# Kernel optimization log

Hardware: AMD Instinct MI355X
Metric: run time of the kernel (lower is better)

Reference implementation:

```python
import jax, jax.numpy as jnp
import numpy as np

B, S, D, H = 4, 4096, 512, 2
PD = D // H  # projection_dim = 256


def setup_inputs() -> dict:
    key = jax.random.key(0)
    ks = jax.random.split(key, 6)
    scale = 1.0 / np.sqrt(D)
    return {
        "x": jax.random.normal(ks[0], (B, S, D), dtype=jnp.float32),
        "Wq": jax.random.normal(ks[1], (D, D), dtype=jnp.float32) * scale,
        "bq": jnp.zeros((D,), dtype=jnp.float32),
        "Wk": jax.random.normal(ks[2], (D, D), dtype=jnp.float32) * scale,
        "bk": jnp.zeros((D,), dtype=jnp.float32),
        "Wv": jax.random.normal(ks[3], (D, D), dtype=jnp.float32) * scale,
        "bv": jnp.zeros((D,), dtype=jnp.float32),
        "Wo": jax.random.normal(ks[4], (D, D), dtype=jnp.float32) * scale,
        "bo": jnp.zeros((D,), dtype=jnp.float32),
    }


def _split_heads(t):
    # [B, S, D] -> [B, H, S, PD]
    return t.reshape(B, S, H, PD).transpose(0, 2, 1, 3)


def reference(x, Wq, bq, Wk, bk, Wv, bv, Wo, bo):
    Q = _split_heads(x @ Wq + bq)
    K = _split_heads(x @ Wk + bk)
    V = _split_heads(x @ Wv + bv)
    # scaled dot-product attention, non-causal (no mask in original)
    scores = jnp.einsum("bhqd,bhkd->bhqk", Q, K) / jnp.sqrt(jnp.float32(PD))
    weights = jax.nn.softmax(scores, axis=-1)
    attn = jnp.einsum("bhqk,bhkd->bhqd", weights, V)
    # merge heads: [B, H, S, PD] -> [B, S, D]
    concat = attn.transpose(0, 2, 1, 3).reshape(B, S, D)
    return concat @ Wo + bo
```

## Files before the change

kernel.cpp:

```cpp
#include <hip/hip_runtime.h>
#include <hip/hip_bf16.h>


#define B_  4
#define S_  4096
#define D_  512
#define H_  2
#define PD_ 256
#define QSCALE 0.09016844f

typedef __attribute__((ext_vector_type(4))) float f32x4;
typedef __attribute__((ext_vector_type(16))) float f32x16;
typedef __attribute__((ext_vector_type(8))) short short8;
typedef __attribute__((ext_vector_type(4))) short short4v;
typedef __attribute__((ext_vector_type(4))) unsigned u32x4;

static __device__ __forceinline__ short f2bf(float f) {
  unsigned u = __float_as_uint(f);
  u += 0x7fffu + ((u >> 16) & 1u);
  return (short)(u >> 16);
}
static __device__ __forceinline__ unsigned cvtpk(float a, float b) {
  unsigned r;
  asm("v_cvt_pk_bf16_f32 %0, %1, %2" : "=v"(r) : "v"(a), "v"(b));
  return r;
}
static __device__ __forceinline__ void gload16(const short* g, const short* l) {
  __builtin_amdgcn_global_load_lds((const __attribute__((address_space(1))) void*)g,
                                   (__attribute__((address_space(3))) void*)l,
                                   16, 0, 0);
}

__global__ void convert_x_kernel(const float* __restrict__ x, short* __restrict__ xb, int n8) {
  int i = blockIdx.x * blockDim.x + threadIdx.x;
  int stride = gridDim.x * blockDim.x;
  for (; i < n8; i += stride) {
    const f32x4* p = (const f32x4*)(x + (size_t)i * 8);
    f32x4 a = p[0], b = p[1];
    short8 v;
    v[0] = f2bf(a[0]); v[1] = f2bf(a[1]); v[2] = f2bf(a[2]); v[3] = f2bf(a[3]);
    v[4] = f2bf(b[0]); v[5] = f2bf(b[1]); v[6] = f2bf(b[2]); v[7] = f2bf(b[3]);
    *(short8*)(xb + (size_t)i * 8) = v;
  }
}

__global__ __launch_bounds__(256) void transpose_w(
    const float* __restrict__ W0, const float* __restrict__ W1,
    const float* __restrict__ W2, const float* __restrict__ W3,
    short* __restrict__ T0, short* __restrict__ T1,
    short* __restrict__ T2, short* __restrict__ T3) {
  const float* W = (blockIdx.z == 0) ? W0 : (blockIdx.z == 1) ? W1 : (blockIdx.z == 2) ? W2 : W3;
  short* T = (blockIdx.z == 0) ? T0 : (blockIdx.z == 1) ? T1 : (blockIdx.z == 2) ? T2 : T3;
  __shared__ float tile[32][33];
  int tx = threadIdx.x & 31, ty = threadIdx.x >> 5;
  int r0 = blockIdx.x * 32, c0 = blockIdx.y * 32;
#pragma unroll
  for (int i = 0; i < 4; ++i)
    tile[ty + 8 * i][tx] = W[(size_t)(r0 + ty + 8 * i) * D_ + c0 + tx];
  __syncthreads();
#pragma unroll
  for (int i = 0; i < 4; ++i)
    T[(size_t)(c0 + ty + 8 * i) * D_ + r0 + tx] = f2bf(tile[tx][ty + 8 * i]);
}

__global__ __launch_bounds__(256) void transpose_v(
    const short* __restrict__ Vw, short* __restrict__ Vt) {
  __shared__ short tile[64][68];
  int h = blockIdx.z;
  int s0 = blockIdx.x * 64, d0 = blockIdx.y * 64;
  const short* src = Vw + (size_t)h * S_ * PD_;
  short* dst = Vt + (size_t)h * S_ * PD_;
  int tx = threadIdx.x & 15, ty = threadIdx.x >> 4;
#pragma unroll
  for (int i = 0; i < 4; ++i) {
    short4v v = *(const short4v*)(src + (size_t)(s0 + ty + 16 * i) * PD_ + d0 + tx * 4);
    *(short4v*)&tile[ty + 16 * i][tx * 4] = v;
  }
  __syncthreads();
#pragma unroll
  for (int i = 0; i < 4; ++i) {
    int d = d0 + ty + 16 * i;
    short4v v;
#pragma unroll
    for (int j = 0; j < 4; ++j) v[j] = tile[tx * 4 + j][ty + 16 * i];
    int swz = ((tx >> 1) & 3) ^ ((d >> 3) & 3);
    *(short4v*)(dst + (size_t)d * S_ + s0 + (tx >> 3) * 32 + swz * 8 + (tx & 1) * 4) = v;
  }
}

template <int MODE>
__global__ __launch_bounds__(256, 2) void gemm_bt(
    const short* __restrict__ A,
    const short* __restrict__ Bt0, const short* __restrict__ Bt1, const short* __restrict__ Bt2,
    const float* __restrict__ b0, const float* __restrict__ b1, const float* __restrict__ b2,
    short* __restrict__ o0, short* __restrict__ o1, short* __restrict__ o2,
    float* __restrict__ fout) {
  __shared__ short sA[128 * 72];
  __shared__ short sB[128 * 72];

  const int tid = threadIdx.x;
  const int lane = tid & 63, wid = tid >> 6;
  const int wr = wid >> 1, wc = wid & 1;
  const int l15 = lane & 15, g = lane >> 4;
  const int m0 = blockIdx.x * 128, n0 = blockIdx.y * 128;

  const short* Bt = (MODE == 0) ? ((blockIdx.z == 0) ? Bt0 : (blockIdx.z == 1) ? Bt1 : Bt2) : Bt0;
  const float* bias = (MODE == 0) ? ((blockIdx.z == 0) ? b0 : (blockIdx.z == 1) ? b1 : b2) : b0;

  short8 pa[4], pb[4];

  auto loadT = [&](int kt) {
#pragma unroll
    for (int i = 0; i < 4; ++i) {
      int slot = tid + 256 * i;
      int r = slot >> 3, gg = slot & 7;
      pa[i] = *(const short8*)(A + (size_t)(m0 + r) * D_ + kt * 64 + 8 * gg);
      pb[i] = *(const short8*)(Bt + (size_t)(n0 + r) * D_ + kt * 64 + 8 * gg);
    }
  };
  auto storeT = [&]() {
#pragma unroll
    for (int i = 0; i < 4; ++i) {
      int slot = tid + 256 * i;
      int r = slot >> 3, gg = slot & 7;
      *(short8*)&sA[r * 72 + 8 * gg] = pa[i];
      *(short8*)&sB[r * 72 + 8 * gg] = pb[i];
    }
  };

  f32x4 acc[4][4];
#pragma unroll
  for (int i = 0; i < 4; ++i)
#pragma unroll
    for (int j = 0; j < 4; ++j) acc[i][j] = (f32x4)0.0f;

  loadT(0);
#pragma unroll 1
  for (int kt = 0; kt < 8; ++kt) {
    __syncthreads();
    storeT();
    if (kt < 7) loadT(kt + 1);
    __syncthreads();
#pragma unroll
    for (int s = 0; s < 2; ++s) {
      short8 a[4], b[4];
#pragma unroll
      for (int fr = 0; fr < 4; ++fr)
        a[fr] = *(const short8*)&sA[(wr * 64 + fr * 16 + l15) * 72 + 32 * s + 8 * g];
#pragma unroll
      for (int fc = 0; fc < 4; ++fc)
        b[fc] = *(const short8*)&sB[(wc * 64 + fc * 16 + l15) * 72 + 32 * s + 8 * g];
#pragma unroll
      for (int fr = 0; fr < 4; ++fr)
#pragma unroll
        for (int fc = 0; fc < 4; ++fc)
          acc[fr][fc] = __builtin_amdgcn_mfma_f32_16x16x32_bf16(a[fr], b[fc], acc[fr][fc], 0, 0, 0);
    }
  }

  if (MODE == 0) {
    short* dst = (blockIdx.z == 0) ? o0 : (blockIdx.z == 1) ? o1 : o2;
    const bool kswz = (blockIdx.z == 1);
    const float sc = (blockIdx.z == 0) ? QSCALE : 1.0f;
#pragma unroll
    for (int fc = 0; fc < 4; ++fc) {
      int n = n0 + wc * 64 + fc * 16 + l15;
      float bvv = bias[n];
      int h = n >> 8, pd = n & 255;
#pragma unroll
      for (int fr = 0; fr < 4; ++fr)
#pragma unroll
        for (int r = 0; r < 4; ++r) {
          int m = m0 + wr * 64 + fr * 16 + 4 * g + r;
          int bb = m >> 12, ss = m & 4095;
          int pdw = pd;
          if (kswz) {
            int ch = pd >> 3;
            pdw = (pd & 7) | (((ch & 24) | ((ch & 7) ^ (ss & 7))) << 3);
          }
          dst[((size_t)((bb * H_ + h) * S_ + ss)) * PD_ + pdw] = f2bf((acc[fr][fc][r] + bvv) * sc);
        }
    }
  } else {
#pragma unroll
    for (int fc = 0; fc < 4; ++fc) {
      int n = n0 + wc * 64 + fc * 16 + l15;
      float bvv = bias[n];
#pragma unroll
      for (int fr = 0; fr < 4; ++fr)
#pragma unroll
        for (int r = 0; r < 4; ++r) {
          int m = m0 + wr * 64 + fr * 16 + 4 * g + r;
          fout[(size_t)m * D_ + n] = acc[fr][fc][r] + bvv;
        }
    }
  }
}

__global__ __launch_bounds__(512, 2) void attn4_kernel(
    const short* __restrict__ Qw, const short* __restrict__ Kw,
    const short* __restrict__ Vt, short* __restrict__ ATT) {
  __shared__ __align__(16) char smem[133120];
  __shared__ float sMm[8][32];
  __shared__ float sB1[8][32];
  __shared__ float sMl[4][32];

  const int tid = threadIdx.x, lane = tid & 63, w = tid >> 6;
  const int l31 = lane & 31, hi = lane >> 5;
  const int head = blockIdx.x & 7, qb = blockIdx.x >> 3;
  const int kh = w >> 2, qg = w & 3;
  const size_t hoff = (size_t)head * S_ * PD_;
  const short* Qh = Qw + hoff;
  const short* Kh = Kw + hoff;
  const short* Vh = Vt + hoff;

  const int qrow = qb * 128 + qg * 32 + l31;
  short8 qf[16];
#pragma unroll
  for (int dc = 0; dc < 16; ++dc)
    qf[dc] = *(const short8*)(Qh + (size_t)qrow * PD_ + dc * 16 + hi * 8);

  const int mm = l31 & 7, pp = (l31 >> 1) & 3, q3 = l31 >> 3;
  int kaddr[4];
#pragma unroll
  for (int b = 0; b < 4; ++b)
    kaddr[b] = kh * 32768 + l31 * 512 + ((b ^ pp) << 5) + ((hi ^ (mm & 1)) << 4);
  int vaddr[2];
#pragma unroll
  for (int c = 0; c < 2; ++c)
    vaddr[c] = 65536 + kh * 32768 + l31 * 64 + (((2 * c + hi) ^ q3) << 4);

  f32x16 o[8];
#pragma unroll
  for (int i = 0; i < 8; ++i) o[i] = (f32x16)0.0f;
  float mrun = -3.0e38f, lrun = 0.0f;

  auto stage = [&](int buf, int t) {
    const short* kt = Kh + (size_t)(t * 32) * PD_;
#pragma unroll
    for (int i = 0; i < 4; ++i) {
      int s = tid + 512 * i;
      int half = s >> 10, s1 = s & 1023;
      gload16(kt + (size_t)(half * 2048) * PD_ + (s1 >> 5) * PD_ + (s1 & 31) * 8,
              (const short*)(smem + half * 32768 + buf * 16384 + s1 * 16));
    }
    const short* vt = Vh + t * 32;
#pragma unroll
    for (int i = 0; i < 4; ++i) {
      int s = tid + 512 * i;
      int half = s >> 10, s1 = s & 1023;
      gload16(vt + (size_t)(s1 >> 2) * S_ + half * 2048 + (s1 & 3) * 8,
              (const short*)(smem + 65536 + half * 32768 + buf * 16384 + s1 * 16));
    }
  };

  auto compute = [&](int buf) {
    f32x16 sa = (f32x16)0.0f, sb = (f32x16)0.0f;
#pragma unroll
    for (int a = 0; a < 4; ++a)
#pragma unroll
      for (int b = 0; b < 4; ++b) {
        short8 kf = *(const short8*)(smem + kaddr[b] + a * 128 + buf * 16384);
        if (a < 2)
          sa = __builtin_amdgcn_mfma_f32_32x32x16_bf16(kf, qf[4 * a + b], sa, 0, 0, 0);
        else
          sb = __builtin_amdgcn_mfma_f32_32x32x16_bf16(kf, qf[4 * a + b], sb, 0, 0, 0);
      }
    f32x16 sacc = sa + sb;

    float tmax = fmaxf(sacc[0], sacc[1]);
#pragma unroll
    for (int r = 2; r < 16; ++r) tmax = fmaxf(tmax, sacc[r]);
    tmax = fmaxf(tmax, __shfl_xor(tmax, 32));
    if (!__all(tmax <= mrun + 8.0f)) {
      float mn = fmaxf(mrun, tmax);
      float resc = exp2f(mrun - mn);
      mrun = mn;
      lrun *= resc;
      if (!hi) sB1[w][l31] = resc;
      asm volatile("" ::: "memory");
      f32x4 rv0 = *(const f32x4*)&sB1[w][0 + hi * 4];
      f32x4 rv1 = *(const f32x4*)&sB1[w][8 + hi * 4];
      f32x4 rv2 = *(const f32x4*)&sB1[w][16 + hi * 4];
      f32x4 rv3 = *(const f32x4*)&sB1[w][24 + hi * 4];
#pragma unroll
      for (int dcb = 0; dcb < 8; ++dcb)
#pragma unroll
        for (int r = 0; r < 16; ++r) {
          float rr = (r < 4 ? rv0 : r < 8 ? rv1 : r < 12 ? rv2 : rv3)[r & 3];
          o[dcb][r] *= rr;
        }
    }
    float lsum = 0.0f;
#pragma unroll
    for (int r = 0; r < 16; ++r) {
      float pv = exp2f(sacc[r] - mrun);
      sacc[r] = pv;
      lsum += pv;
    }
    lsum += __shfl_xor(lsum, 32);
    lrun += lsum;

#pragma unroll
    for (int c = 0; c < 2; ++c) {
      unsigned pk0 = cvtpk(sacc[8 * c + 0], sacc[8 * c + 1]);
      unsigned pk1 = cvtpk(sacc[8 * c + 2], sacc[8 * c + 3]);
      unsigned pk2 = cvtpk(sacc[8 * c + 4], sacc[8 * c + 5]);
      unsigned pk3 = cvtpk(sacc[8 * c + 6], sacc[8 * c + 7]);
      unsigned sh0 = __shfl_xor(pk0, 32);
      unsigned sh1 = __shfl_xor(pk1, 32);
      unsigned sh2 = __shfl_xor(pk2, 32);
      unsigned sh3 = __shfl_xor(pk3, 32);
      u32x4 ua;
      ua[0] = hi ? sh2 : pk0;
      ua[1] = hi ? sh3 : pk1;
      ua[2] = hi ? pk2 : sh0;
      ua[3] = hi ? pk3 : sh1;
      short8 af = *(short8*)&ua;
#pragma unroll
      for (int dcb = 0; dcb < 8; ++dcb) {
        short8 vf = *(const short8*)(smem + vaddr[c] + dcb * 2048 + buf * 16384);
        o[dcb] = __builtin_amdgcn_mfma_f32_32x32x16_bf16(af, vf, o[dcb], 0, 0, 0);
      }
    }
  };

  stage(0, 0);
#pragma unroll 1
  for (int t = 0; t < 64; t += 2) {
    __syncthreads();
    stage(1, t + 1);
    compute(0);
    __syncthreads();
    if (t + 2 < 64) stage(0, t + 2);
    compute(1);
  }

  __syncthreads();
  if (!hi) sMm[w][l31] = mrun;
  __syncthreads();
  {
    float mo = sMm[w ^ 4][l31];
    float mf = fmaxf(mrun, mo);
    float sc = exp2f(mrun - mf);
    lrun *= sc;
    if (!hi) sB1[w][l31] = sc;
    asm volatile("" ::: "memory");
    f32x4 rv0 = *(const f32x4*)&sB1[w][0 + hi * 4];
    f32x4 rv1 = *(const f32x4*)&sB1[w][8 + hi * 4];
    f32x4 rv2 = *(const f32x4*)&sB1[w][16 + hi * 4];
    f32x4 rv3 = *(const f32x4*)&sB1[w][24 + hi * 4];
#pragma unroll
    for (int dcb = 0; dcb < 8; ++dcb)
#pragma unroll
      for (int r = 0; r < 16; ++r) {
        float rr = (r < 4 ? rv0 : r < 8 ? rv1 : r < 12 ? rv2 : rv3)[r & 3];
        o[dcb][r] *= rr;
      }
    if (w >= 4 && !hi) sMl[w - 4][l31] = lrun;
  }
  __syncthreads();
  float* mb = (float*)smem;
  if (w >= 4) {
    float* rg = mb + (size_t)qg * 8320;
#pragma unroll
    for (int dcb = 0; dcb < 8; ++dcb)
#pragma unroll
      for (int r4 = 0; r4 < 4; ++r4) {
        f32x4 v;
        v[0] = o[dcb][4 * r4 + 0];
        v[1] = o[dcb][4 * r4 + 1];
        v[2] = o[dcb][4 * r4 + 2];
        v[3] = o[dcb][4 * r4 + 3];
        *(f32x4*)&rg[(size_t)(dcb * 4 + r4) * 260 + lane * 4] = v;
      }
  }
  __syncthreads();
  if (w < 4) {
    float* rg = mb + (size_t)qg * 8320;
#pragma unroll
    for (int dcb = 0; dcb < 8; ++dcb)
#pragma unroll
      for (int r4 = 0; r4 < 4; ++r4) {
        f32x4 v = *(const f32x4*)&rg[(size_t)(dcb * 4 + r4) * 260 + lane * 4];
        o[dcb][4 * r4 + 0] += v[0];
        o[dcb][4 * r4 + 1] += v[1];
        o[dcb][4 * r4 + 2] += v[2];
        o[dcb][4 * r4 + 3] += v[3];
      }
    lrun += sMl[qg][l31];
    if (!hi) sB1[w][l31] = 1.0f / lrun;
    asm volatile("" ::: "memory");
    f32x4 iv0 = *(const f32x4*)&sB1[w][0 + hi * 4];
    f32x4 iv1 = *(const f32x4*)&sB1[w][8 + hi * 4];
    f32x4 iv2 = *(const f32x4*)&sB1[w][16 + hi * 4];
    f32x4 iv3 = *(const f32x4*)&sB1[w][24 + hi * 4];
    const int bb = head >> 1, hh = head & 1;
#pragma unroll
    for (int r = 0; r < 16; ++r) {
      int q = qb * 128 + qg * 32 + (r & 3) + 8 * (r >> 2) + 4 * hi;
      float iv = (r < 4 ? iv0 : r < 8 ? iv1 : r < 12 ? iv2 : iv3)[r & 3];
      size_t base = ((size_t)(bb * S_ + q)) * D_ + hh * PD_;
#pragma unroll
      for (int dcb = 0; dcb < 8; ++dcb)
        ATT[base + dcb * 32 + l31] = f2bf(o[dcb][r] * iv);
    }
  }
}

extern "C" void kernel_launch(void* const* d_in, const int* in_sizes, int n_in,
                              void* d_out, int out_size, void* d_ws, size_t ws_size,
                              hipStream_t stream) {
  const float* x  = (const float*)d_in[0];
  const float* Wq = (const float*)d_in[1];
  const float* bq = (const float*)d_in[2];
  const float* Wk = (const float*)d_in[3];
  const float* bk = (const float*)d_in[4];
  const float* Wv = (const float*)d_in[5];
  const float* bv = (const float*)d_in[6];
  const float* Wo = (const float*)d_in[7];
  const float* bo = (const float*)d_in[8];
  float* out = (float*)d_out;

  char* ws = (char*)d_ws;
  const size_t WSZ = (size_t)D_ * D_ * 2;
  const size_t QSZ = (size_t)B_ * H_ * S_ * PD_ * 2;
  short* wtq = (short*)(ws);
  short* wtk = (short*)(ws + WSZ);
  short* wtv = (short*)(ws + 2 * WSZ);
  short* wto = (short*)(ws + 3 * WSZ);
  short* Qw  = (short*)(ws + 4 * WSZ);
  short* Kw  = (short*)(ws + 4 * WSZ + QSZ);
  short* Vw  = (short*)(ws + 4 * WSZ + 2 * QSZ);
  short* ATT = (short*)(ws + 4 * WSZ + 3 * QSZ);
  short* XB  = ATT;
  short* Vtp = (short*)d_out;

  convert_x_kernel<<<dim3(2048), dim3(256), 0, stream>>>(x, XB, (B_ * S_ * D_) / 8);
  transpose_w<<<dim3(16, 16, 4), dim3(256), 0, stream>>>(Wq, Wk, Wv, Wo, wtq, wtk, wtv, wto);
  gemm_bt<0><<<dim3(128, 4, 3), dim3(256), 0, stream>>>(
      XB, wtq, wtk, wtv, bq, bk, bv, Qw, Kw, Vw, (float*)nullptr);
  transpose_v<<<dim3(64, 4, 8), dim3(256), 0, stream>>>(Vw, Vtp);
  attn4_kernel<<<dim3(256), dim3(512), 0, stream>>>(Qw, Kw, Vtp, ATT);
  gemm_bt<1><<<dim3(128, 4, 1), dim3(256), 0, stream>>>(
      ATT, wto, wto, wto, bo, bo, bo, nullptr, nullptr, nullptr, out);
}
```

Measured before the change: 290.2 us.

## Software-pipeline attention: overlap next QK^T with current softmax and PV

Restructures the attention main loop so the QK^T MFMAs for the next key tile are issued before the softmax and PV of the previous tile, using double-buffered K and triple-buffered V in a larger LDS allocation. There is one barrier per tile instead of two. MFMA sections are wrapped in s_setprio to favour matrix issue, and row-rescale factors are broadcast with lane shuffles instead of LDS round-trips. This aims to hide softmax latency and barrier stalls behind matrix work. The cost is more registers for two score accumulators and 160KB of LDS, which risks occupancy or spills under the 2-block launch bound.

```diff
diff --git a/kernel.cpp b/kernel.cpp
--- a/kernel.cpp
+++ b/kernel.cpp
@@ -197,13 +197,10 @@
   }
 }
 
-__global__ __launch_bounds__(512, 2) void attn4_kernel(
+__global__ __launch_bounds__(512, 2) void attn6_kernel(
     const short* __restrict__ Qw, const short* __restrict__ Kw,
     const short* __restrict__ Vt, short* __restrict__ ATT) {
-  __shared__ __align__(16) char smem[133120];
-  __shared__ float sMm[8][32];
-  __shared__ float sB1[8][32];
-  __shared__ float sMl[4][32];
+  __shared__ __align__(16) char smem[163840];
 
   const int tid = threadIdx.x, lane = tid & 63, w = tid >> 6;
   const int l31 = lane & 31, hi = lane >> 5;
@@ -211,7 +208,6 @@
   const int kh = w >> 2, qg = w & 3;
   const size_t hoff = (size_t)head * S_ * PD_;
   const short* Qh = Qw + hoff;
-  const short* Kh = Kw + hoff;
   const short* Vh = Vt + hoff;
 
   const int qrow = qb * 128 + qg * 32 + l31;
@@ -224,188 +220,205 @@
   int kaddr[4];
 #pragma unroll
   for (int b = 0; b < 4; ++b)
-    kaddr[b] = kh * 32768 + l31 * 512 + ((b ^ pp) << 5) + ((hi ^ (mm & 1)) << 4);
+    kaddr[b] = kh * 16384 + l31 * 512 + ((b ^ pp) << 5) + ((hi ^ (mm & 1)) << 4);
   int vaddr[2];
 #pragma unroll
   for (int c = 0; c < 2; ++c)
-    vaddr[c] = 65536 + kh * 32768 + l31 * 64 + (((2 * c + hi) ^ q3) << 4);
+    vaddr[c] = kh * 16384 + l31 * 64 + (((2 * c + hi) ^ q3) << 4);
+
+  const int lk0 = tid * 16;
+  const int gk0 = (tid >> 5) * PD_ + (tid & 31) * 8;
+  const int gv0 = (tid >> 2) * S_ + (tid & 3) * 8;
+  const short* kg = Kw + hoff;
+  const short* vg = Vh;
 
   f32x16 o[8];
 #pragma unroll
   for (int i = 0; i < 8; ++i) o[i] = (f32x16)0.0f;
+  f32x16 sA, sB;
   float mrun = -3.0e38f, lrun = 0.0f;
 
-  auto stage = [&](int buf, int t) {
-    const short* kt = Kh + (size_t)(t * 32) * PD_;
-#pragma unroll
-    for (int i = 0; i < 4; ++i) {
-      int s = tid + 512 * i;
-      int half = s >> 10, s1 = s & 1023;
-      gload16(kt + (size_t)(half * 2048) * PD_ + (s1 >> 5) * PD_ + (s1 & 31) * 8,
-              (const short*)(smem + half * 32768 + buf * 16384 + s1 * 16));
-    }
-    const short* vt = Vh + t * 32;
-#pragma unroll
-    for (int i = 0; i < 4; ++i) {
-      int s = tid + 512 * i;
-      int half = s >> 10, s1 = s & 1023;
-      gload16(vt + (size_t)(s1 >> 2) * S_ + half * 2048 + (s1 & 3) * 8,
-              (const short*)(smem + 65536 + half * 32768 + buf * 16384 + s1 * 16));
-    }
-  };
-
-  auto compute = [&](int buf) {
-    f32x16 sa = (f32x16)0.0f, sb = (f32x16)0.0f;
-#pragma unroll
-    for (int a = 0; a < 4; ++a)
-#pragma unroll
-      for (int b = 0; b < 4; ++b) {
-        short8 kf = *(const short8*)(smem + kaddr[b] + a * 128 + buf * 16384);
-        if (a < 2)
-          sa = __builtin_amdgcn_mfma_f32_32x32x16_bf16(kf, qf[4 * a + b], sa, 0, 0, 0);
-        else
-          sb = __builtin_amdgcn_mfma_f32_32x32x16_bf16(kf, qf[4 * a + b], sb, 0, 0, 0);
-      }
-    f32x16 sacc = sa + sb;
-
-    float tmax = fmaxf(sacc[0], sacc[1]);
-#pragma unroll
-    for (int r = 2; r < 16; ++r) tmax = fmaxf(tmax, sacc[r]);
-    tmax = fmaxf(tmax, __shfl_xor(tmax, 32));
-    if (!__all(tmax <= mrun + 8.0f)) {
-      float mn = fmaxf(mrun, tmax);
-      float resc = exp2f(mrun - mn);
-      mrun = mn;
-      lrun *= resc;
-      if (!hi) sB1[w][l31] = resc;
-      asm volatile("" ::: "memory");
-      f32x4 rv0 = *(const f32x4*)&sB1[w][0 + hi * 4];
-      f32x4 rv1 = *(const f32x4*)&sB1[w][8 + hi * 4];
-      f32x4 rv2 = *(const f32x4*)&sB1[w][16 + hi * 4];
-      f32x4 rv3 = *(const f32x4*)&sB1[w][24 + hi * 4];
-#pragma unroll
-      for (int dcb = 0; dcb < 8; ++dcb)
-#pragma unroll
-        for (int r = 0; r < 16; ++r) {
-          float rr = (r < 4 ? rv0 : r < 8 ? rv1 : r < 12 ? rv2 : rv3)[r & 3];
-          o[dcb][r] *= rr;
-        }
-    }
-    float lsum = 0.0f;
-#pragma unroll
-    for (int r = 0; r < 16; ++r) {
-      float pv = exp2f(sacc[r] - mrun);
-      sacc[r] = pv;
-      lsum += pv;
-    }
-    lsum += __shfl_xor(lsum, 32);
-    lrun += lsum;
-
-#pragma unroll
-    for (int c = 0; c < 2; ++c) {
-      unsigned pk0 = cvtpk(sacc[8 * c + 0], sacc[8 * c + 1]);
-      unsigned pk1 = cvtpk(sacc[8 * c + 2], sacc[8 * c + 3]);
-      unsigned pk2 = cvtpk(sacc[8 * c + 4], sacc[8 * c + 5]);
-      unsigned pk3 = cvtpk(sacc[8 * c + 6], sacc[8 * c + 7]);
-      unsigned sh0 = __shfl_xor(pk0, 32);
-      unsigned sh1 = __shfl_xor(pk1, 32);
-      unsigned sh2 = __shfl_xor(pk2, 32);
-      unsigned sh3 = __shfl_xor(pk3, 32);
-      u32x4 ua;
-      ua[0] = hi ? sh2 : pk0;
-      ua[1] = hi ? sh3 : pk1;
-      ua[2] = hi ? pk2 : sh0;
-      ua[3] = hi ? pk3 : sh1;
-      short8 af = *(short8*)&ua;
-#pragma unroll
-      for (int dcb = 0; dcb < 8; ++dcb) {
-        short8 vf = *(const short8*)(smem + vaddr[c] + dcb * 2048 + buf * 16384);
-        o[dcb] = __builtin_amdgcn_mfma_f32_32x32x16_bf16(af, vf, o[dcb], 0, 0, 0);
-      }
-    }
-  };
-
-  stage(0, 0);
+#define STAGE_K(KN)                                                                  \
+  gload16(kg + gk0,          (const short*)(smem + (KN) * 32768 + lk0));             \
+  gload16(kg + gk0 + 4096,   (const short*)(smem + (KN) * 32768 + 8192 + lk0));      \
+  gload16(kg + gk0 + 524288, (const short*)(smem + (KN) * 32768 + 16384 + lk0));     \
+  gload16(kg + gk0 + 528384, (const short*)(smem + (KN) * 32768 + 24576 + lk0));
+
+#define STAGE_V(VS)                                                                  \
+  gload16(vg + gv0,          (const short*)(smem + 65536 + (VS) * 32768 + lk0));     \
+  gload16(vg + gv0 + 524288, (const short*)(smem + 65536 + (VS) * 32768 + 8192 + lk0)); \
+  gload16(vg + gv0 + 2048,   (const short*)(smem + 65536 + (VS) * 32768 + 16384 + lk0)); \
+  gload16(vg + gv0 + 526336, (const short*)(smem + 65536 + (VS) * 32768 + 24576 + lk0));
+
+#define QK_(SCUR, KC)                                                                \
+  {                                                                                  \
+    f32x16 _a = (f32x16)0.0f, _b = (f32x16)0.0f;                                     \
+    __builtin_amdgcn_s_setprio(1);                                                   \
+    _Pragma("unroll")                                                                \
+    for (int a = 0; a < 4; ++a) {                                                    \
+      _Pragma("unroll")                                                              \
+      for (int b = 0; b < 4; ++b) {                                                  \
+        short8 kf = *(const short8*)(smem + (KC) * 32768 + kaddr[b] + a * 128);      \
+        if (b & 1) _b = __builtin_amdgcn_mfma_f32_32x32x16_bf16(kf, qf[4 * a + b], _b, 0, 0, 0); \
+        else       _a = __builtin_amdgcn_mfma_f32_32x32x16_bf16(kf, qf[4 * a + b], _a, 0, 0, 0); \
+      }                                                                              \
+    }                                                                                \
+    __builtin_amdgcn_s_setprio(0);                                                   \
+    SCUR = _a + _b;                                                                  \
+  }
+
+#define SM_(S)                                                                       \
+  {                                                                                  \
+    float t0 = fmaxf(S[0], S[1]),   t1 = fmaxf(S[2], S[3]);                          \
+    float t2 = fmaxf(S[4], S[5]),   t3 = fmaxf(S[6], S[7]);                          \
+    float t4 = fmaxf(S[8], S[9]),   t5 = fmaxf(S[10], S[11]);                        \
+    float t6 = fmaxf(S[12], S[13]), t7 = fmaxf(S[14], S[15]);                        \
+    t0 = fmaxf(t0, t1); t2 = fmaxf(t2, t3); t4 = fmaxf(t4, t5); t6 = fmaxf(t6, t7);  \
+    t0 = fmaxf(t0, t2); t4 = fmaxf(t4, t6);                                          \
+    float tmax = fmaxf(t0, t4);                                                      \
+    tmax = fmaxf(tmax, __shfl_xor(tmax, 32));                                        \
+    if (!__all(tmax <= mrun + 8.0f)) {                                               \
+      float mn = fmaxf(mrun, tmax);                                                  \
+      float resc = exp2f(mrun - mn);                                                 \
+      mrun = mn; lrun *= resc;                                                       \
+      _Pragma("unroll")                                                              \
+      for (int r = 0; r < 16; ++r) {                                                 \
+        float rr = __shfl(resc, (r & 3) + 8 * (r >> 2) + 4 * hi, 64);                \
+        _Pragma("unroll")                                                            \
+        for (int d = 0; d < 8; ++d) o[d][r] *= rr;                                   \
+      }                                                                              \
+    }                                                                                \
+    _Pragma("unroll")                                                                \
+    for (int r = 0; r < 16; ++r) S[r] = exp2f(S[r] - mrun);                          \
+    float u0 = (S[0] + S[1]) + (S[2] + S[3]);                                        \
+    float u1 = (S[4] + S[5]) + (S[6] + S[7]);                                        \
+    u0 += (S[8] + S[9]) + (S[10] + S[11]);                                           \
+    u1 += (S[12] + S[13]) + (S[14] + S[15]);                                         \
+    float ls = u0 + u1;                                                              \
+    ls += __shfl_xor(ls, 32);                                                        \
+    lrun += ls;                                                                      \
+  }
+
+#define PV_(S, VP)                                                                   \
+  {                                                                                  \
+    _Pragma("unroll")                                                                \
+    for (int c = 0; c < 2; ++c) {                                                    \
+      unsigned pk0 = cvtpk(S[8 * c + 0], S[8 * c + 1]);                              \
+      unsigned pk1 = cvtpk(S[8 * c + 2], S[8 * c + 3]);                              \
+      unsigned pk2 = cvtpk(S[8 * c + 4], S[8 * c + 5]);                              \
+      unsigned pk3 = cvtpk(S[8 * c + 6], S[8 * c + 7]);                              \
+      unsigned sh0 = __shfl_xor(pk0, 32);                                            \
+      unsigned sh1 = __shfl_xor(pk1, 32);                                            \
+      unsigned sh2 = __shfl_xor(pk2, 32);                                            \
+      unsigned sh3 = __shfl_xor(pk3, 32);                                            \
+      u32x4 ua;                                                                      \
+      ua[0] = hi ? sh2 : pk0;                                                        \
+      ua[1] = hi ? sh3 : pk1;                                                        \
+      ua[2] = hi ? pk2 : sh0;                                                        \
+      ua[3] = hi ? pk3 : sh1;                                                        \
+      short8 af = *(short8*)&ua;                                                     \
+      __builtin_amdgcn_s_setprio(1);                                                 \
+      _Pragma("unroll")                                                              \
+      for (int d = 0; d < 8; ++d) {                                                  \
+        short8 vf = *(const short8*)(smem + 65536 + (VP) * 32768 + vaddr[c] + d * 2048); \
+        o[d] = __builtin_amdgcn_mfma_f32_32x32x16_bf16(af, vf, o[d], 0, 0, 0);       \
+      }                                                                              \
+      __builtin_amdgcn_s_setprio(0);                                                 \
+    }                                                                                \
+  }
+
+#define REGION(KC, KN, VP, VS, SCUR, SPRV, DOSTAGE)                                  \
+  __syncthreads();                                                                   \
+  if (DOSTAGE) { STAGE_K(KN); STAGE_V(VS); }                                         \
+  kg += 32 * PD_; vg += 32;                                                          \
+  QK_(SCUR, KC);                                                                     \
+  SM_(SPRV);                                                                         \
+  PV_(SPRV, VP);
+
+  STAGE_K(0); STAGE_V(0);
+  kg += 32 * PD_; vg += 32;
+  __syncthreads();
+  STAGE_K(1); STAGE_V(1);
+  kg += 32 * PD_; vg += 32;
+  QK_(sA, 0);
+
 #pragma unroll 1
-  for (int t = 0; t < 64; t += 2) {
-    __syncthreads();
-    stage(1, t + 1);
-    compute(0);
-    __syncthreads();
-    if (t + 2 < 64) stage(0, t + 2);
-    compute(1);
-  }
-
-  __syncthreads();
-  if (!hi) sMm[w][l31] = mrun;
+  for (int it = 0; it < 10; ++it) {
+    REGION(1, 0, 0, 2, sB, sA, 1)
+    REGION(0, 1, 1, 0, sA, sB, 1)
+    REGION(1, 0, 2, 1, sB, sA, 1)
+    REGION(0, 1, 0, 2, sA, sB, 1)
+    REGION(1, 0, 1, 0, sB, sA, 1)
+    REGION(0, 1, 2, 1, sA, sB, 1)
+  }
+  REGION(1, 0, 0, 2, sB, sA, 1)
+  REGION(0, 1, 1, 0, sA, sB, 1)
+  REGION(1, 0, 2, 1, sB, sA, 0)
+  SM_(sB);
+  PV_(sB, 0);
+
+  __syncthreads();
+  float* sMm = (float*)smem;
+  float* sMl = (float*)(smem + 1024);
+  float* dep = (float*)(smem + 4096);
+  if (!hi) sMm[w * 32 + l31] = mrun;
   __syncthreads();
   {
-    float mo = sMm[w ^ 4][l31];
+    float mo = sMm[(w ^ 4) * 32 + l31];
     float mf = fmaxf(mrun, mo);
     float sc = exp2f(mrun - mf);
     lrun *= sc;
-    if (!hi) sB1[w][l31] = sc;
-    asm volatile("" ::: "memory");
-    f32x4 rv0 = *(const f32x4*)&sB1[w][0 + hi * 4];
-    f32x4 rv1 = *(const f32x4*)&sB1[w][8 + hi * 4];
-    f32x4 rv2 = *(const f32x4*)&sB1[w][16 + hi * 4];
-    f32x4 rv3 = *(const f32x4*)&sB1[w][24 + hi * 4];
-#pragma unroll
-    for (int dcb = 0; dcb < 8; ++dcb)
-#pragma unroll
-      for (int r = 0; r < 16; ++r) {
-        float rr = (r < 4 ? rv0 : r < 8 ? rv1 : r < 12 ? rv2 : rv3)[r & 3];
-        o[dcb][r] *= rr;
-      }
-    if (w >= 4 && !hi) sMl[w - 4][l31] = lrun;
-  }
-  __syncthreads();
-  float* mb = (float*)smem;
+#pragma unroll
+    for (int r = 0; r < 16; ++r) {
+      float rr = __shfl(sc, (r & 3) + 8 * (r >> 2) + 4 * hi, 64);
+#pragma unroll
+      for (int d = 0; d < 8; ++d) o[d][r] *= rr;
+    }
+    if (w >= 4 && !hi) sMl[(w - 4) * 32 + l31] = lrun;
+  }
+  __syncthreads();
   if (w >= 4) {
-    float* rg = mb + (size_t)qg * 8320;
-#pragma unroll
-    for (int dcb = 0; dcb < 8; ++dcb)
+    float* rg = dep + (size_t)qg * 8320;
+#pragma unroll
+    for (int d = 0; d < 8; ++d)
 #pragma unroll
       for (int r4 = 0; r4 < 4; ++r4) {
         f32x4 v;
-        v[0] = o[dcb][4 * r4 + 0];
-        v[1] = o[dcb][4 * r4 + 1];
-        v[2] = o[dcb][4 * r4 + 2];
-        v[3] = o[dcb][4 * r4 + 3];
-        *(f32x4*)&rg[(size_t)(dcb * 4 + r4) * 260 + lane * 4] = v;
+#pragma unroll
+        for (int j = 0; j < 4; ++j) v[j] = o[d][4 * r4 + j];
+        *(f32x4*)&rg[(size_t)(d * 4 + r4) * 260 + lane * 4] = v;
       }
   }
   __syncthreads();
   if (w < 4) {
-    float* rg = mb + (size_t)qg * 8320;
-#pragma unroll
-    for (int dcb = 0; dcb < 8; ++dcb)
+    float* rg = dep + (size_t)qg * 8320;
+#pragma unroll
+    for (int d = 0; d < 8; ++d)
 #pragma unroll
       for (int r4 = 0; r4 < 4; ++r4) {
-        f32x4 v = *(const f32x4*)&rg[(size_t)(dcb * 4 + r4) * 260 + lane * 4];
-        o[dcb][4 * r4 + 0] += v[0];
-        o[dcb][4 * r4 + 1] += v[1];
-        o[dcb][4 * r4 + 2] += v[2];
-        o[dcb][4 * r4 + 3] += v[3];
+        f32x4 v = *(const f32x4*)&rg[(size_t)(d * 4 + r4) * 260 + lane * 4];
+#pragma unroll
+        for (int j = 0; j < 4; ++j) o[d][4 * r4 + j] += v[j];
       }
-    lrun += sMl[qg][l31];
-    if (!hi) sB1[w][l31] = 1.0f / lrun;
-    asm volatile("" ::: "memory");
-    f32x4 iv0 = *(const f32x4*)&sB1[w][0 + hi * 4];
-    f32x4 iv1 = *(const f32x4*)&sB1[w][8 + hi * 4];
-    f32x4 iv2 = *(const f32x4*)&sB1[w][16 + hi * 4];
-    f32x4 iv3 = *(const f32x4*)&sB1[w][24 + hi * 4];
+    lrun += sMl[qg * 32 + l31];
+    float inv = 1.0f / lrun;
     const int bb = head >> 1, hh = head & 1;
 #pragma unroll
     for (int r = 0; r < 16; ++r) {
       int q = qb * 128 + qg * 32 + (r & 3) + 8 * (r >> 2) + 4 * hi;
-      float iv = (r < 4 ? iv0 : r < 8 ? iv1 : r < 12 ? iv2 : iv3)[r & 3];
+      float iv = __shfl(inv, (r & 3) + 8 * (r >> 2) + 4 * hi, 64);
       size_t base = ((size_t)(bb * S_ + q)) * D_ + hh * PD_;
 #pragma unroll
-      for (int dcb = 0; dcb < 8; ++dcb)
-        ATT[base + dcb * 32 + l31] = f2bf(o[dcb][r] * iv);
-    }
-  }
+      for (int d = 0; d < 8; ++d)
+        ATT[base + d * 32 + l31] = f2bf(o[d][r] * iv);
+    }
+  }
+#undef STAGE_K
+#undef STAGE_V
+#undef QK_
+#undef SM_
+#undef PV_
+#undef REGION
 }
 
 extern "C" void kernel_launch(void* const* d_in, const int* in_sizes, int n_in,
@@ -441,7 +454,7 @@
   gemm_bt<0><<<dim3(128, 4, 3), dim3(256), 0, stream>>>(
       XB, wtq, wtk, wtv, bq, bk, bv, Qw, Kw, Vw, (float*)nullptr);
   transpose_v<<<dim3(64, 4, 8), dim3(256), 0, stream>>>(Vw, Vtp);
-  attn4_kernel<<<dim3(256), dim3(512), 0, stream>>>(Qw, Kw, Vtp, ATT);
+  attn6_kernel<<<dim3(256), dim3(512), 0, stream>>>(Qw, Kw, Vtp, ATT);
   gemm_bt<1><<<dim3(128, 4, 1), dim3(256), 0, stream>>>(
       ATT, wto, wto, wto, bo, bo, bo, nullptr, nullptr, nullptr, out);
 }
```

Result: slower. 488.5 us (+68.3%).
